# Kernel optimization log

Hardware: AMD Instinct MI355X
Metric: run time of the kernel (lower is better)

## Reference

```python
import jax, jax.numpy as jnp
import numpy as np

MAX_NUM_CAPS = 10
NEG = -1e9

def _layernorm(x, g, b):
    m = x.mean(-1, keepdims=True)
    v = x.var(-1, keepdims=True)
    return (x - m) / jnp.sqrt(v + 1e-5) * g + b

def _gatv2(x, Wl, Wr, att, bias, adj):
    # x: [B,M,F]; Wl/Wr: [F,H*C]; att: [H,C]; adj: [B,M,M] bool, adj[b,i,j] = edge i->j
    B, M, F = x.shape
    H, C = att.shape
    xl = jnp.einsum('bmf,fhc->bmhc', x, Wl.reshape(F, H, C))  # source transform
    xr = jnp.einsum('bmf,fhc->bmhc', x, Wr.reshape(F, H, C))  # target transform
    # GATv2 score: att . leaky_relu(xl[i] + xr[j]) for edge (src=i, dst=j)
    z = jax.nn.leaky_relu(xl[:, :, None, :, :] + xr[:, None, :, :, :], 0.2)  # [B,i,j,H,C]
    e = jnp.einsum('bijhc,hc->bijh', z, att)
    e = jnp.where(adj[..., None], e, NEG)
    alpha = jax.nn.softmax(e, axis=1)  # softmax over incoming sources i per target j
    out = jnp.einsum('bijh,bihc->bjhc', alpha, xl)  # aggregate at targets
    return out.reshape(B, M, H * C) + bias

def setup_inputs() -> dict:
    key = jax.random.key(0)
    ks = jax.random.split(key, 16)
    B, N, T = 128, 16, 48
    Fm, H, C3 = 128, 4, 64
    s = 0.05
    inp = {
        'team_obs': jax.random.normal(ks[0], (B, N, 14), jnp.float32),
        'target_obs': jax.random.normal(ks[1], (B, T, 15), jnp.float32),
        'team_mask': jax.random.normal(ks[2], (B, 2, N), jnp.float32),
        'local_target_mask': jnp.ones((B, T + 1), jnp.float32),
        'W_emb': jax.random.normal(ks[3], (16, Fm), jnp.float32) * s,
        'b_emb': jnp.zeros((Fm,), jnp.float32),
        'Wl1': jax.random.normal(ks[4], (Fm, Fm), jnp.float32) * s,
        'Wr1': jax.random.normal(ks[5], (Fm, Fm), jnp.float32) * s,
        'att1': jax.random.normal(ks[6], (H, Fm // H), jnp.float32) * s,
        'b1': jnp.zeros((Fm,), jnp.float32),
        'Wl2': jax.random.normal(ks[7], (Fm, Fm), jnp.float32) * s,
        'Wr2': jax.random.normal(ks[8], (Fm, Fm), jnp.float32) * s,
        'att2': jax.random.normal(ks[9], (H, Fm // H), jnp.float32) * s,
        'b2': jnp.zeros((Fm,), jnp.float32),
        'Wl3': jax.random.normal(ks[10], (Fm, C3), jnp.float32) * s,
        'Wr3': jax.random.normal(ks[11], (Fm, C3), jnp.float32) * s,
        'att3': jax.random.normal(ks[12], (1, C3), jnp.float32) * s,
        'b3': jnp.zeros((C3,), jnp.float32),
        'ln1_g': jnp.ones((Fm,), jnp.float32),
        'ln1_b': jnp.zeros((Fm,), jnp.float32),
        'ln2_g': jnp.ones((Fm,), jnp.float32),
        'ln2_b': jnp.zeros((Fm,), jnp.float32),
    }
    return inp

def reference(team_obs, target_obs, team_mask, local_target_mask,
              W_emb, b_emb, Wl1, Wr1, att1, b1, Wl2, Wr2, att2, b2,
              Wl3, Wr3, att3, b3, ln1_g, ln1_b, ln2_g, ln2_b):
    B, N, _ = team_obs.shape
    team = jnp.concatenate([team_obs, jnp.zeros((B, N, 2), team_obs.dtype)], axis=2)
    tgt = target_obs[:, :, :-1]
    T = tgt.shape[1]
    tgt = jnp.concatenate([tgt[:, :, :2 + MAX_NUM_CAPS],
                           jnp.zeros((B, T, 2), tgt.dtype),
                           tgt[:, :, -2:]], axis=2)
    fin = jnp.concatenate([team, tgt], axis=1)  # [B, M, inp_dim]
    h = fin @ W_emb + b_emb  # [B, M, 128]
    imp_team = team_mask[:, 0] != -1e9          # [B, N]
    imp_tgt = local_target_mask[:, :-1] != 0.0  # [B, T]
    imp = jnp.concatenate([imp_team, imp_tgt], axis=1)  # [B, M]
    M = N + T
    eye = jnp.eye(M, dtype=bool)
    # edges among active nodes minus diagonal; PyG GATv2Conv add_self_loops=True re-adds self edges
    adj = (imp[:, :, None] & imp[:, None, :] & ~eye) | eye  # [B, M, M]
    out = jax.nn.relu(_layernorm(_gatv2(h, Wl1, Wr1, att1, b1, adj), ln1_g, ln1_b))
    out = jax.nn.relu(_layernorm(_gatv2(out, Wl2, Wr2, att2, b2, adj), ln2_g, ln2_b))
    out = _gatv2(out, Wl3, Wr3, att3, b3, adj)
    return out  # [B, M, out_dim]
```

## Files before the change

### kernel.cpp

```cpp
#include <hip/hip_runtime.h>

typedef unsigned short u16;
typedef unsigned int   u32;
typedef _Float16 h2  __attribute__((ext_vector_type(2)));
typedef __fp16   hw2 __attribute__((ext_vector_type(2)));
typedef __fp16   hw8 __attribute__((ext_vector_type(8)));
typedef float    f4  __attribute__((ext_vector_type(4)));

#define XS 136
#define PS 72
#define BS 72
#define OS 72

static __device__ __forceinline__ h2 pk(float a, float b) {
    return __builtin_bit_cast(h2, __builtin_amdgcn_cvt_pkrtz(a, b));
}
static __device__ __forceinline__ float dot2(h2 a, h2 b, float c) {
    return __builtin_amdgcn_fdot2(__builtin_bit_cast(hw2, a),
                                  __builtin_bit_cast(hw2, b), c, false);
}
static __device__ __forceinline__ h2  b2h(u32 v) { return __builtin_bit_cast(h2, v); }
static __device__ __forceinline__ u32 h2u(h2 v)  { return __builtin_bit_cast(u32, v); }
static __device__ __forceinline__ h2  abs2(h2 v) { return b2h(h2u(v) & 0x7fff7fffu); }
static __device__ __forceinline__ u16 f2h(float f) { return __builtin_bit_cast(u16, (_Float16)f); }
static __device__ __forceinline__ f4 mfma16(uint4 a, uint4 b, f4 c) {
    return __builtin_amdgcn_mfma_f32_16x16x32_f16(__builtin_bit_cast(hw8, a),
                                                  __builtin_bit_cast(hw8, b), c, 0, 0, 0);
}

__global__ void pack_weights(const float* __restrict__ Wl1, const float* __restrict__ Wr1,
                             const float* __restrict__ Wl2, const float* __restrict__ Wr2,
                             const float* __restrict__ Wl3, const float* __restrict__ Wr3,
                             u32* __restrict__ wpk)
{
    const int o = blockIdx.x * 256 + threadIdx.x;
    const float* src; u32* dst; int local; int N;
    if      (o < 8192)  { src = Wl1; dst = wpk;         local = o;         N = 128; }
    else if (o < 16384) { src = Wr1; dst = wpk + 8192;  local = o - 8192;  N = 128; }
    else if (o < 24576) { src = Wl2; dst = wpk + 16384; local = o - 16384; N = 128; }
    else if (o < 32768) { src = Wr2; dst = wpk + 24576; local = o - 24576; N = 128; }
    else if (o < 36864) { src = Wl3; dst = wpk + 32768; local = o - 32768; N = 64;  }
    else                { src = Wr3; dst = wpk + 36864; local = o - 36864; N = 64;  }
    const int i2   = local & 3;
    const int lane = (local >> 2) & 63;
    const int frag = local >> 8;
    const int kb   = frag & 3;
    const int nt   = frag >> 2;
    const int k0   = kb*32 + ((lane >> 4) << 3) + i2*2;
    const int n    = nt*16 + (lane & 15);
    dst[local] = h2u(pk(src[k0*N + n], src[(k0+1)*N + n]));
}

static __device__ __forceinline__ void compute_imp(int t, int b,
    const float* __restrict__ team_mask, const float* __restrict__ ltm, float* sImp)
{
    if (t < 64) {
        float im;
        if (t < 16) im = (team_mask[b*32 + t] != -1000000000.0f) ? 1.f : 0.f;
        else        im = (ltm[b*49 + (t-16)] != 0.0f) ? 1.f : 0.f;
        sImp[t] = im;
    }
}

static __device__ __forceinline__ void matmul128(int w, int lane,
    const u32* __restrict__ wpkL, const u32* __restrict__ wpkR,
    const u16* sX, u16* sXl, uint4* sXrP, u16* sXlB)
{
    const int  mt  = w & 3;
    const bool isR = (w >> 2) & 1;
    const int  nh  = w >> 3;
    const u32* wp  = isR ? wpkR : wpkL;
    const int  n15 = lane & 15;
    const int  qd  = lane >> 4;
    uint4 afr[4];
#pragma unroll
    for (int kb = 0; kb < 4; kb++)
        afr[kb] = *(const uint4*)&sX[(mt*16 + n15)*XS + kb*32 + (qd << 3)];
#pragma unroll
    for (int nt = nh*4; nt < nh*4 + 4; nt++) {
        f4 acc = {0.f, 0.f, 0.f, 0.f};
#pragma unroll
        for (int kb = 0; kb < 4; kb++) {
            uint4 bf = *(const uint4*)&wp[((nt*4 + kb)*64 + lane)*4];
            acc = mfma16(afr[kb], bf, acc);
        }
        const int n  = nt*16 + n15;
        const int mb = mt*16 + (qd << 2);
        if (!isR) {
#pragma unroll
            for (int r = 0; r < 4; r++) sXl[(mb + r)*XS + n] = f2h(acc[r]);
            uint2 u;
            u.x = h2u(pk(acc[0], acc[1]));
            u.y = h2u(pk(acc[2], acc[3]));
            *(uint2*)&sXlB[n*BS + mb] = u;
        } else {
            u16* xp = (u16*)sXrP;
#pragma unroll
            for (int r = 0; r < 4; r++)
                xp[(((n >> 3)*64) + mb + r)*8 + (n & 7)] = f2h(acc[r]);
        }
    }
}

static __device__ __forceinline__ void attn_scores(int w, int lane,
    const float* __restrict__ att,
    const u16* sXl, const uint4* sXrP, u16* sP,
    float* sAl, float* sL2, const float* sImp)
{
    const int h  = w & 3;
    const int qf = w >> 2;
    const int j  = lane;

    h2 a2[16];
#pragma unroll
    for (int q = 0; q < 16; q++) a2[q] = pk(att[h*32 + 2*q], att[h*32 + 2*q + 1]);

    if (w < 4) {
        const uint4* pr = (const uint4*)&sXl[lane*XS + h*32];
        float al = 0.f;
#pragma unroll
        for (int c4 = 0; c4 < 4; c4++) {
            uint4 v = pr[c4];
            al = dot2(b2h(v.x), a2[c4*4+0], al);
            al = dot2(b2h(v.y), a2[c4*4+1], al);
            al = dot2(b2h(v.z), a2[c4*4+2], al);
            al = dot2(b2h(v.w), a2[c4*4+3], al);
        }
        sAl[h*64 + lane] = al;
    }

    h2 xr2[16];
#pragma unroll
    for (int s = 0; s < 4; s++) {
        uint4 v = sXrP[(h*4 + s)*64 + j];
        xr2[s*4+0] = b2h(v.x); xr2[s*4+1] = b2h(v.y);
        xr2[s*4+2] = b2h(v.z); xr2[s*4+3] = b2h(v.w);
    }
    float Ar = 0.f;
#pragma unroll
    for (int q = 0; q < 16; q++) Ar = dot2(a2[q], xr2[q], Ar);
    const float impj = sImp[j];
    __syncthreads();

    float l = 0.f;
    uint4* pd = (uint4*)&sP[(h*64 + j)*PS + qf*16];
    for (int c8 = 0; c8 < 2; c8++) {
        u32 pr4[4];
        float pprev = 0.f;
#pragma unroll
        for (int i2 = 0; i2 < 8; i2++) {
            const int i = qf*16 + c8*8 + i2;
            const uint4* pl = (const uint4*)&sXl[i*XS + h*32];
            uint4 v0 = pl[0], v1 = pl[1], v2 = pl[2], v3 = pl[3];
            h2 xl2[16];
            xl2[0] = b2h(v0.x); xl2[1] = b2h(v0.y); xl2[2]  = b2h(v0.z); xl2[3]  = b2h(v0.w);
            xl2[4] = b2h(v1.x); xl2[5] = b2h(v1.y); xl2[6]  = b2h(v1.z); xl2[7]  = b2h(v1.w);
            xl2[8] = b2h(v2.x); xl2[9] = b2h(v2.y); xl2[10] = b2h(v2.z); xl2[11] = b2h(v2.w);
            xl2[12]= b2h(v3.x); xl2[13]= b2h(v3.y); xl2[14] = b2h(v3.z); xl2[15] = b2h(v3.w);
            float S0 = 0.f, S1 = 0.f;
#pragma unroll
            for (int q = 0; q < 16; q += 2) {
                h2 t0 = abs2(xl2[q]   + xr2[q]);
                h2 t1 = abs2(xl2[q+1] + xr2[q+1]);
                S0 = dot2(a2[q],   t0, S0);
                S1 = dot2(a2[q+1], t1, S1);
            }
            float e  = 0.6f*(sAl[h*64 + i] + Ar) + 0.4f*(S0 + S1);
            float ad = (i == j) ? 1.f : impj * sImp[i];
            float p  = (ad != 0.f) ? __expf(e) : 0.f;
            if (i2 & 1) {
                h2 pp = pk(pprev, p);
                pr4[i2 >> 1] = h2u(pp);
                l += (float)pp[0] + (float)pp[1];
            } else {
                pprev = p;
            }
        }
        pd[c8] = make_uint4(pr4[0], pr4[1], pr4[2], pr4[3]);
    }
    sL2[h*256 + qf*64 + j] = l;
}

static __device__ __forceinline__ void attn_agg_ln(int w, int lane,
    const float* __restrict__ bias, const float* __restrict__ lg, const float* __restrict__ lb,
    const u16* sP, const u16* sXlB, float* sOutF, const float* sL2,
    float* sPart, u16* sXout)
{
    const int h   = w & 3;
    const int jq  = w >> 2;
    const int n15 = lane & 15;
    const int kq  = lane >> 4;

    f4 acc0 = {0.f,0.f,0.f,0.f}, acc1 = acc0;
#pragma unroll
    for (int ks = 0; ks < 2; ks++) {
        uint4 af  = *(const uint4*)&sP[(h*64 + jq*16 + n15)*PS + ks*32 + kq*8];
        uint4 bf0 = *(const uint4*)&sXlB[(h*32 +  0 + n15)*BS + ks*32 + kq*8];
        uint4 bf1 = *(const uint4*)&sXlB[(h*32 + 16 + n15)*BS + ks*32 + kq*8];
        acc0 = mfma16(af, bf0, acc0);
        acc1 = mfma16(af, bf1, acc1);
    }
    {
        const int jb0 = jq*16 + kq*4;
#pragma unroll
        for (int r = 0; r < 4; r++) {
            sOutF[(h*32 +  0 + n15)*OS + jb0 + r] = acc0[r];
            sOutF[(h*32 + 16 + n15)*OS + jb0 + r] = acc1[r];
        }
    }
    __syncthreads();

    const int cg = w, j = lane, hd = cg >> 2;
    const float l  = (sL2[hd*256 + j]       + sL2[hd*256 +  64 + j])
                   + (sL2[hd*256 + 128 + j] + sL2[hd*256 + 192 + j]);
    const float rl = 1.f / l;
    float y[8];
    float s1 = 0.f, s2 = 0.f;
#pragma unroll
    for (int k = 0; k < 8; k++) {
        float v = fmaf(sOutF[(cg*8 + k)*OS + j], rl, bias[cg*8 + k]);
        y[k] = v; s1 += v; s2 = fmaf(v, v, s2);
    }
    sPart[cg*64 + j]        = s1;
    sPart[1024 + cg*64 + j] = s2;
    __syncthreads();
    float su = 0.f, sq = 0.f;
#pragma unroll
    for (int p = 0; p < 16; p++) { su += sPart[p*64 + j]; sq += sPart[1024 + p*64 + j]; }
    const float mean = su * 0.0078125f;
    const float var  = sq * 0.0078125f - mean*mean;
    const float rstd = rsqrtf(var + 1e-5f);
    u32* xo = (u32*)&sXout[j*XS];
#pragma unroll
    for (int q = 0; q < 4; q++) {
        const int c0 = cg*8 + 2*q;
        float v0 = fmaxf(fmaf((y[2*q]   - mean)*rstd, lg[c0],   lb[c0]),   0.f);
        float v1 = fmaxf(fmaf((y[2*q+1] - mean)*rstd, lg[c0+1], lb[c0+1]), 0.f);
        xo[cg*4 + q] = h2u(pk(v0, v1));
    }
}

__global__ void __launch_bounds__(1024, 4) gnn_fused(
    const float* __restrict__ team_obs, const float* __restrict__ target_obs,
    const float* __restrict__ team_mask, const float* __restrict__ ltm,
    const float* __restrict__ W_emb, const float* __restrict__ b_emb,
    const float* __restrict__ att1, const float* __restrict__ b1,
    const float* __restrict__ ln1_g, const float* __restrict__ ln1_b,
    const float* __restrict__ att2, const float* __restrict__ b2,
    const float* __restrict__ ln2_g, const float* __restrict__ ln2_b,
    const float* __restrict__ att3, const float* __restrict__ b3,
    const u32* __restrict__ wpk, float* __restrict__ out)
{
    __shared__ __align__(16) u16   sX  [64*XS];
    __shared__ __align__(16) u16   sXl [64*XS];
    __shared__ __align__(16) uint4 sXrP[1024];
    __shared__ __align__(16) u16   sXlB[128*BS];
    __shared__ __align__(16) u16   sP  [4*64*PS];
    __shared__ __align__(16) float sOutF[128*OS];
    __shared__ float sAl [256];
    __shared__ float sPart[2048];
    __shared__ float sL2 [1024];
    __shared__ float sImp[64];

    const int t    = threadIdx.x;
    const int w    = t >> 6;
    const int lane = t & 63;
    const int b    = blockIdx.x;

    float* sFin = (float*)sP;

    compute_imp(t, b, team_mask, ltm, sImp);
    {
        int m = t >> 4, k = t & 15;
        float v = 0.f;
        if (m < 16) {
            if (k < 14) v = team_obs[(b*16 + m)*14 + k];
        } else {
            const float* tg = target_obs + (size_t)(b*48 + (m-16))*15;
            if      (k < 12)  v = tg[k];
            else if (k == 14) v = tg[12];
            else if (k == 15) v = tg[13];
        }
        sFin[m*16 + k] = v;
    }
    __syncthreads();

    {
        const int f = t & 127;
        const int g = t >> 7;
        float wreg[16];
#pragma unroll
        for (int k = 0; k < 16; k++) wreg[k] = W_emb[k*128 + f];
        const float bf = b_emb[f];
#pragma unroll
        for (int mm = 0; mm < 8; mm++) {
            int m = g*8 + mm;
            const float4* pf = (const float4*)&sFin[m*16];
            float4 f0 = pf[0], f1 = pf[1], f2 = pf[2], f3 = pf[3];
            float acc = bf;
            acc = fmaf(f0.x, wreg[0],  acc); acc = fmaf(f0.y, wreg[1],  acc);
            acc = fmaf(f0.z, wreg[2],  acc); acc = fmaf(f0.w, wreg[3],  acc);
            acc = fmaf(f1.x, wreg[4],  acc); acc = fmaf(f1.y, wreg[5],  acc);
            acc = fmaf(f1.z, wreg[6],  acc); acc = fmaf(f1.w, wreg[7],  acc);
            acc = fmaf(f2.x, wreg[8],  acc); acc = fmaf(f2.y, wreg[9],  acc);
            acc = fmaf(f2.z, wreg[10], acc); acc = fmaf(f2.w, wreg[11], acc);
            acc = fmaf(f3.x, wreg[12], acc); acc = fmaf(f3.y, wreg[13], acc);
            acc = fmaf(f3.z, wreg[14], acc); acc = fmaf(f3.w, wreg[15], acc);
            sX[m*XS + f] = f2h(acc);
        }
    }
    __syncthreads();

    matmul128(w, lane, wpk, wpk + 8192, sX, sXl, sXrP, sXlB);
    __syncthreads();
    attn_scores(w, lane, att1, sXl, sXrP, sP, sAl, sL2, sImp);
    __syncthreads();
    attn_agg_ln(w, lane, b1, ln1_g, ln1_b, sP, sXlB, sOutF, sL2, sPart, sX);
    __syncthreads();

    matmul128(w, lane, wpk + 16384, wpk + 24576, sX, sXl, sXrP, sXlB);
    __syncthreads();
    attn_scores(w, lane, att2, sXl, sXrP, sP, sAl, sL2, sImp);
    __syncthreads();
    attn_agg_ln(w, lane, b2, ln2_g, ln2_b, sP, sXlB, sOutF, sL2, sPart, sX);
    __syncthreads();

    {
        const int  mt  = w & 3;
        const bool isR = (w >> 2) & 1;
        const int  nh  = w >> 3;
        const u32* wp  = isR ? (wpk + 36864) : (wpk + 32768);
        const int  n15 = lane & 15;
        const int  qd  = lane >> 4;
        uint4 afr[4];
#pragma unroll
        for (int kb = 0; kb < 4; kb++)
            afr[kb] = *(const uint4*)&sX[(mt*16 + n15)*XS + kb*32 + (qd << 3)];
#pragma unroll
        for (int nt = nh*2; nt < nh*2 + 2; nt++) {
            f4 acc = {0.f, 0.f, 0.f, 0.f};
#pragma unroll
            for (int kb = 0; kb < 4; kb++) {
                uint4 bf = *(const uint4*)&wp[((nt*4 + kb)*64 + lane)*4];
                acc = mfma16(afr[kb], bf, acc);
            }
            const int n  = nt*16 + n15;
            const int mb = mt*16 + (qd << 2);
            if (!isR) {
#pragma unroll
                for (int r = 0; r < 4; r++) sXl[(mb + r)*XS + n] = f2h(acc[r]);
                uint2 u;
                u.x = h2u(pk(acc[0], acc[1]));
                u.y = h2u(pk(acc[2], acc[3]));
                *(uint2*)&sXlB[n*BS + mb] = u;
            } else {
                u16* xp = (u16*)sXrP;
#pragma unroll
                for (int r = 0; r < 4; r++)
                    xp[(((n >> 3)*64) + mb + r)*8 + (n & 7)] = f2h(acc[r]);
            }
        }
    }
    __syncthreads();

    {
        h2 a2l[2];
        a2l[0] = pk(att3[w*4 + 0], att3[w*4 + 1]);
        a2l[1] = pk(att3[w*4 + 2], att3[w*4 + 3]);
        uint2 v = *(const uint2*)&sXl[lane*XS + w*4];
        float al = dot2(b2h(v.x), a2l[0], 0.f);
        al = dot2(b2h(v.y), a2l[1], al);
        sPart[w*64 + lane] = al;
    }
    __syncthreads();
    if (t < 64) {
        float s = 0.f;
#pragma unroll
        for (int p = 0; p < 16; p += 4)
            s += ((sPart[p*64 + t] + sPart[(p+1)*64 + t]) +
                  (sPart[(p+2)*64 + t] + sPart[(p+3)*64 + t]));
        sAl[t] = s;
    }
    __syncthreads();

    {
        h2 a3[32], xr3[32];
#pragma unroll
        for (int q = 0; q < 32; q++) a3[q] = pk(att3[2*q], att3[2*q + 1]);
#pragma unroll
        for (int s = 0; s < 8; s++) {
            uint4 v = sXrP[s*64 + lane];
            xr3[s*4+0] = b2h(v.x); xr3[s*4+1] = b2h(v.y);
            xr3[s*4+2] = b2h(v.z); xr3[s*4+3] = b2h(v.w);
        }
        float Ar = 0.f;
#pragma unroll
        for (int q = 0; q < 32; q++) Ar = dot2(a3[q], xr3[q], Ar);
        const float impj = sImp[lane];
        float l3 = 0.f;
        u32 pr2[2];
        float pprev = 0.f;
#pragma unroll
        for (int ii = 0; ii < 4; ii++) {
            const int i = w*4 + ii;
            const uint4* pl = (const uint4*)&sXl[i*XS];
            float S0 = 0.f, S1 = 0.f;
#pragma unroll
            for (int c4 = 0; c4 < 8; c4++) {
                uint4 v = pl[c4];
                S0 = dot2(a3[c4*4+0], abs2(b2h(v.x) + xr3[c4*4+0]), S0);
                S1 = dot2(a3[c4*4+1], abs2(b2h(v.y) + xr3[c4*4+1]), S1);
                S0 = dot2(a3[c4*4+2], abs2(b2h(v.z) + xr3[c4*4+2]), S0);
                S1 = dot2(a3[c4*4+3], abs2(b2h(v.w) + xr3[c4*4+3]), S1);
            }
            float e  = 0.6f*(sAl[i] + Ar) + 0.4f*(S0 + S1);
            float ad = (i == lane) ? 1.f : impj * sImp[i];
            float p  = (ad != 0.f) ? __expf(e) : 0.f;
            if (ii & 1) {
                h2 pp = pk(pprev, p);
                pr2[ii >> 1] = h2u(pp);
                l3 += (float)pp[0] + (float)pp[1];
            } else {
                pprev = p;
            }
        }
        *(uint2*)&sP[lane*PS + w*4] = make_uint2(pr2[0], pr2[1]);
        sPart[w*64 + lane] = l3;
    }
    __syncthreads();
    if (t < 64) {
        float s = 0.f;
#pragma unroll
        for (int p = 0; p < 16; p += 4)
            s += ((sPart[p*64 + t] + sPart[(p+1)*64 + t]) +
                  (sPart[(p+2)*64 + t] + sPart[(p+3)*64 + t]));
        sL2[t] = 1.f / s;
    }

    {
        const int jt  = w & 3;
        const int ct  = w >> 2;
        const int n15 = lane & 15;
        const int kq  = lane >> 4;
        f4 acc = {0.f,0.f,0.f,0.f};
#pragma unroll
        for (int ks = 0; ks < 2; ks++) {
            uint4 af = *(const uint4*)&sP[(jt*16 + n15)*PS + ks*32 + kq*8];
            uint4 bf = *(const uint4*)&sXlB[(ct*16 + n15)*BS + ks*32 + kq*8];
            acc = mfma16(af, bf, acc);
        }
        __syncthreads();
        const int c  = ct*16 + n15;
        const float bc = b3[c];
#pragma unroll
        for (int r = 0; r < 4; r++) {
            const int jj = jt*16 + kq*4 + r;
            out[(size_t)b*4096 + (size_t)jj*64 + c] = fmaf(acc[r], sL2[jj], bc);
        }
    }
}

extern "C" void kernel_launch(void* const* d_in, const int* in_sizes, int n_in,
                              void* d_out, int out_size, void* d_ws, size_t ws_size,
                              hipStream_t stream) {
    (void)in_sizes; (void)n_in; (void)ws_size; (void)out_size;
    const float* team_obs          = (const float*)d_in[0];
    const float* target_obs        = (const float*)d_in[1];
    const float* team_mask         = (const float*)d_in[2];
    const float* local_target_mask = (const float*)d_in[3];
    const float* W_emb             = (const float*)d_in[4];
    const float* b_emb             = (const float*)d_in[5];
    const float* Wl1               = (const float*)d_in[6];
    const float* Wr1               = (const float*)d_in[7];
    const float* att1              = (const float*)d_in[8];
    const float* b1                = (const float*)d_in[9];
    const float* Wl2               = (const float*)d_in[10];
    const float* Wr2               = (const float*)d_in[11];
    const float* att2              = (const float*)d_in[12];
    const float* b2                = (const float*)d_in[13];
    const float* Wl3               = (const float*)d_in[14];
    const float* Wr3               = (const float*)d_in[15];
    const float* att3              = (const float*)d_in[16];
    const float* b3                = (const float*)d_in[17];
    const float* ln1_g             = (const float*)d_in[18];
    const float* ln1_b             = (const float*)d_in[19];
    const float* ln2_g             = (const float*)d_in[20];
    const float* ln2_b             = (const float*)d_in[21];
    float* out = (float*)d_out;

    u32* wpk = (u32*)d_ws;

    pack_weights<<<dim3(160), dim3(256), 0, stream>>>(Wl1, Wr1, Wl2, Wr2, Wl3, Wr3, wpk);
    gnn_fused<<<dim3(128), dim3(1024), 0, stream>>>(
        team_obs, target_obs, team_mask, local_target_mask, W_emb, b_emb,
        att1, b1, ln1_g, ln1_b, att2, b2, ln2_g, ln2_b, att3, b3, wpk, out);
}
```

Measured before the change: 133.9 us.

## Replace shared-memory reductions and barriers with wavefront shuffles in attention and layernorm

Each wave now computes its own per-source attention term and broadcasts it with __shfl instead of staging it in shared memory, which removes a block barrier in each attention-score pass and two in layer 3. The aggregation/layernorm step keeps the MFMA accumulators in registers and reduces row statistics with xor-shuffles plus a small shared partial buffer, dropping the sOutF staging buffer and one barrier. The cost is redundant dot-product work per wave, and shared memory use shrinks, which could allow more resident blocks.

After: 138.9 us. +3.8%, slower.

```diff
diff --git a/kernel.cpp b/kernel.cpp
--- a/kernel.cpp
+++ b/kernel.cpp
@@ -10,7 +10,6 @@
 #define XS 136
 #define PS 72
 #define BS 72
-#define OS 72
 
 static __device__ __forceinline__ h2 pk(float a, float b) {
     return __builtin_bit_cast(h2, __builtin_amdgcn_cvt_pkrtz(a, b));
@@ -105,7 +104,7 @@
 static __device__ __forceinline__ void attn_scores(int w, int lane,
     const float* __restrict__ att,
     const u16* sXl, const uint4* sXrP, u16* sP,
-    float* sAl, float* sL2, const float* sImp)
+    float* sL2, const float* sImp)
 {
     const int h  = w & 3;
     const int qf = w >> 2;
@@ -115,9 +114,11 @@
 #pragma unroll
     for (int q = 0; q < 16; q++) a2[q] = pk(att[h*32 + 2*q], att[h*32 + 2*q + 1]);
 
-    if (w < 4) {
-        const uint4* pr = (const uint4*)&sXl[lane*XS + h*32];
-        float al = 0.f;
+    float al;
+    {
+        const int ia = qf*16 + (lane & 15);
+        const uint4* pr = (const uint4*)&sXl[ia*XS + h*32];
+        al = 0.f;
 #pragma unroll
         for (int c4 = 0; c4 < 4; c4++) {
             uint4 v = pr[c4];
@@ -126,7 +127,6 @@
             al = dot2(b2h(v.z), a2[c4*4+2], al);
             al = dot2(b2h(v.w), a2[c4*4+3], al);
         }
-        sAl[h*64 + lane] = al;
     }
 
     h2 xr2[16];
@@ -140,7 +140,6 @@
 #pragma unroll
     for (int q = 0; q < 16; q++) Ar = dot2(a2[q], xr2[q], Ar);
     const float impj = sImp[j];
-    __syncthreads();
 
     float l = 0.f;
     uint4* pd = (uint4*)&sP[(h*64 + j)*PS + qf*16];
@@ -149,7 +148,8 @@
         float pprev = 0.f;
 #pragma unroll
         for (int i2 = 0; i2 < 8; i2++) {
-            const int i = qf*16 + c8*8 + i2;
+            const int idx = c8*8 + i2;
+            const int i   = qf*16 + idx;
             const uint4* pl = (const uint4*)&sXl[i*XS + h*32];
             uint4 v0 = pl[0], v1 = pl[1], v2 = pl[2], v3 = pl[3];
             h2 xl2[16];
@@ -165,7 +165,8 @@
                 S0 = dot2(a2[q],   t0, S0);
                 S1 = dot2(a2[q+1], t1, S1);
             }
-            float e  = 0.6f*(sAl[h*64 + i] + Ar) + 0.4f*(S0 + S1);
+            const float Al_i = __shfl(al, idx);
+            float e  = 0.6f*(Al_i + Ar) + 0.4f*(S0 + S1);
             float ad = (i == j) ? 1.f : impj * sImp[i];
             float p  = (ad != 0.f) ? __expf(e) : 0.f;
             if (i2 & 1) {
@@ -183,7 +184,7 @@
 
 static __device__ __forceinline__ void attn_agg_ln(int w, int lane,
     const float* __restrict__ bias, const float* __restrict__ lg, const float* __restrict__ lb,
-    const u16* sP, const u16* sXlB, float* sOutF, const float* sL2,
+    const u16* sP, const u16* sXlB, const float* sL2,
     float* sPart, u16* sXout)
 {
     const int h   = w & 3;
@@ -200,43 +201,53 @@
         acc0 = mfma16(af, bf0, acc0);
         acc1 = mfma16(af, bf1, acc1);
     }
-    {
-        const int jb0 = jq*16 + kq*4;
+    const int c0 = h*32 + n15, c1 = c0 + 16;
+    const float bc0 = bias[c0], bc1 = bias[c1];
+    float y0[4], y1[4], s1v[4], s2v[4];
+#pragma unroll
+    for (int r = 0; r < 4; r++) {
+        const int jr = jq*16 + kq*4 + r;
+        const float lr = (sL2[h*256 + jr]       + sL2[h*256 +  64 + jr])
+                       + (sL2[h*256 + 128 + jr] + sL2[h*256 + 192 + jr]);
+        const float rl = 1.f / lr;
+        y0[r] = fmaf(acc0[r], rl, bc0);
+        y1[r] = fmaf(acc1[r], rl, bc1);
+        s1v[r] = y0[r] + y1[r];
+        s2v[r] = fmaf(y0[r], y0[r], y1[r]*y1[r]);
+    }
+#pragma unroll
+    for (int off = 1; off < 16; off <<= 1) {
 #pragma unroll
         for (int r = 0; r < 4; r++) {
-            sOutF[(h*32 +  0 + n15)*OS + jb0 + r] = acc0[r];
-            sOutF[(h*32 + 16 + n15)*OS + jb0 + r] = acc1[r];
-        }
-    }
-    __syncthreads();
-
-    const int cg = w, j = lane, hd = cg >> 2;
-    const float l  = (sL2[hd*256 + j]       + sL2[hd*256 +  64 + j])
-                   + (sL2[hd*256 + 128 + j] + sL2[hd*256 + 192 + j]);
-    const float rl = 1.f / l;
-    float y[8];
-    float s1 = 0.f, s2 = 0.f;
-#pragma unroll
-    for (int k = 0; k < 8; k++) {
-        float v = fmaf(sOutF[(cg*8 + k)*OS + j], rl, bias[cg*8 + k]);
-        y[k] = v; s1 += v; s2 = fmaf(v, v, s2);
-    }
-    sPart[cg*64 + j]        = s1;
-    sPart[1024 + cg*64 + j] = s2;
-    __syncthreads();
-    float su = 0.f, sq = 0.f;
-#pragma unroll
-    for (int p = 0; p < 16; p++) { su += sPart[p*64 + j]; sq += sPart[1024 + p*64 + j]; }
-    const float mean = su * 0.0078125f;
-    const float var  = sq * 0.0078125f - mean*mean;
-    const float rstd = rsqrtf(var + 1e-5f);
-    u32* xo = (u32*)&sXout[j*XS];
-#pragma unroll
-    for (int q = 0; q < 4; q++) {
-        const int c0 = cg*8 + 2*q;
-        float v0 = fmaxf(fmaf((y[2*q]   - mean)*rstd, lg[c0],   lb[c0]),   0.f);
-        float v1 = fmaxf(fmaf((y[2*q+1] - mean)*rstd, lg[c0+1], lb[c0+1]), 0.f);
-        xo[cg*4 + q] = h2u(pk(v0, v1));
+            s1v[r] += __shfl_xor(s1v[r], off);
+            s2v[r] += __shfl_xor(s2v[r], off);
+        }
+    }
+    if (n15 == 0) {
+#pragma unroll
+        for (int r = 0; r < 4; r++) {
+            const int jr = jq*16 + kq*4 + r;
+            sPart[jr*8 + h]     = s1v[r];
+            sPart[jr*8 + 4 + h] = s2v[r];
+        }
+    }
+    __syncthreads();
+
+    const float g0 = lg[c0], g1 = lg[c1], e0 = lb[c0], e1 = lb[c1];
+#pragma unroll
+    for (int r = 0; r < 4; r++) {
+        const int jr = jq*16 + kq*4 + r;
+        const float4 sv1 = *(const float4*)&sPart[jr*8];
+        const float4 sv2 = *(const float4*)&sPart[jr*8 + 4];
+        const float su = (sv1.x + sv1.y) + (sv1.z + sv1.w);
+        const float sq = (sv2.x + sv2.y) + (sv2.z + sv2.w);
+        const float mean = su * 0.0078125f;
+        const float var  = sq * 0.0078125f - mean*mean;
+        const float rstd = rsqrtf(var + 1e-5f);
+        float v0 = fmaxf(fmaf((y0[r] - mean)*rstd, g0, e0), 0.f);
+        float v1 = fmaxf(fmaf((y1[r] - mean)*rstd, g1, e1), 0.f);
+        sXout[jr*XS + c0] = f2h(v0);
+        sXout[jr*XS + c1] = f2h(v1);
     }
 }
 
@@ -256,9 +267,7 @@
     __shared__ __align__(16) uint4 sXrP[1024];
     __shared__ __align__(16) u16   sXlB[128*BS];
     __shared__ __align__(16) u16   sP  [4*64*PS];
-    __shared__ __align__(16) float sOutF[128*OS];
-    __shared__ float sAl [256];
-    __shared__ float sPart[2048];
+    __shared__ float sPart[1024];
     __shared__ float sL2 [1024];
     __shared__ float sImp[64];
 
@@ -313,16 +322,16 @@
 
     matmul128(w, lane, wpk, wpk + 8192, sX, sXl, sXrP, sXlB);
     __syncthreads();
-    attn_scores(w, lane, att1, sXl, sXrP, sP, sAl, sL2, sImp);
-    __syncthreads();
-    attn_agg_ln(w, lane, b1, ln1_g, ln1_b, sP, sXlB, sOutF, sL2, sPart, sX);
+    attn_scores(w, lane, att1, sXl, sXrP, sP, sL2, sImp);
+    __syncthreads();
+    attn_agg_ln(w, lane, b1, ln1_g, ln1_b, sP, sXlB, sL2, sPart, sX);
     __syncthreads();
 
     matmul128(w, lane, wpk + 16384, wpk + 24576, sX, sXl, sXrP, sXlB);
     __syncthreads();
-    attn_scores(w, lane, att2, sXl, sXrP, sP, sAl, sL2, sImp);
-    __syncthreads();
-    attn_agg_ln(w, lane, b2, ln2_g, ln2_b, sP, sXlB, sOutF, sL2, sPart, sX);
+    attn_scores(w, lane, att2, sXl, sXrP, sP, sL2, sImp);
+    __syncthreads();
+    attn_agg_ln(w, lane, b2, ln2_g, ln2_b, sP, sXlB, sL2, sPart, sX);
     __syncthreads();
 
     {
@@ -364,29 +373,23 @@
     __syncthreads();
 
     {
-        h2 a2l[2];
-        a2l[0] = pk(att3[w*4 + 0], att3[w*4 + 1]);
-        a2l[1] = pk(att3[w*4 + 2], att3[w*4 + 3]);
-        uint2 v = *(const uint2*)&sXl[lane*XS + w*4];
-        float al = dot2(b2h(v.x), a2l[0], 0.f);
-        al = dot2(b2h(v.y), a2l[1], al);
-        sPart[w*64 + lane] = al;
-    }
-    __syncthreads();
-    if (t < 64) {
-        float s = 0.f;
-#pragma unroll
-        for (int p = 0; p < 16; p += 4)
-            s += ((sPart[p*64 + t] + sPart[(p+1)*64 + t]) +
-                  (sPart[(p+2)*64 + t] + sPart[(p+3)*64 + t]));
-        sAl[t] = s;
-    }
-    __syncthreads();
-
-    {
         h2 a3[32], xr3[32];
 #pragma unroll
         for (int q = 0; q < 32; q++) a3[q] = pk(att3[2*q], att3[2*q + 1]);
+        float al3;
+        {
+            const int ia = w*4 + (lane & 3);
+            const uint4* pl = (const uint4*)&sXl[ia*XS];
+            al3 = 0.f;
+#pragma unroll
+            for (int c4 = 0; c4 < 8; c4++) {
+                uint4 v = pl[c4];
+                al3 = dot2(b2h(v.x), a3[c4*4+0], al3);
+                al3 = dot2(b2h(v.y), a3[c4*4+1], al3);
+                al3 = dot2(b2h(v.z), a3[c4*4+2], al3);
+                al3 = dot2(b2h(v.w), a3[c4*4+3], al3);
+            }
+        }
 #pragma unroll
         for (int s = 0; s < 8; s++) {
             uint4 v = sXrP[s*64 + lane];
@@ -413,7 +416,8 @@
                 S0 = dot2(a3[c4*4+2], abs2(b2h(v.z) + xr3[c4*4+2]), S0);
                 S1 = dot2(a3[c4*4+3], abs2(b2h(v.w) + xr3[c4*4+3]), S1);
             }
-            float e  = 0.6f*(sAl[i] + Ar) + 0.4f*(S0 + S1);
+            const float Al_i = __shfl(al3, ii);
+            float e  = 0.6f*(Al_i + Ar) + 0.4f*(S0 + S1);
             float ad = (i == lane) ? 1.f : impj * sImp[i];
             float p  = (ad != 0.f) ? __expf(e) : 0.f;
             if (ii & 1) {
```
